# Kernel tuning notes

Hardware: AMD Instinct MI355X
Metric: run time of the kernel (lower is better)

The kernel has to match this reference:

```python
import jax, jax.numpy as jnp
import numpy as np

S, T, C, L_GNN, L_TF, H = 8, 16, 128, 3, 2, 4
B = 512
FF = 4 * C
EPS = 1e-5


def setup_inputs() -> dict:
    key = jax.random.key(0)
    ks = jax.random.split(key, 24)
    w = lambda k, shape: jax.random.normal(k, shape, jnp.float32) * 0.05
    inp = {}
    inp["xx"] = jax.random.randint(ks[0], (B, T, S, S, S), 0, 3, dtype=jnp.int32)
    inp["ss"] = jax.random.uniform(ks[1], (B, 1), jnp.float32)
    # DynamicGNNv2 params
    inp["Win"] = w(ks[2], (C, 5)); inp["b_in"] = w(ks[3], (C,))
    inp["Wl"] = w(ks[4], (L_GNN, C, C)); inp["bl"] = w(ks[5], (L_GNN, C))   # SAGEConv lin_l (neighbors)
    inp["Wr"] = w(ks[6], (L_GNN, C, C))                                      # SAGEConv lin_r (root, no bias)
    inp["ln_g"] = jnp.ones((C,), jnp.float32); inp["ln_b"] = jnp.zeros((C,), jnp.float32)  # shared LayerNorm
    # TransformerEncoder params (norm_first, relu, dropout=0 at eval)
    inp["Wqkv"] = w(ks[7], (L_TF, 3 * C, C)); inp["bqkv"] = w(ks[8], (L_TF, 3 * C))
    inp["Wo"] = w(ks[9], (L_TF, C, C)); inp["bo"] = w(ks[10], (L_TF, C))
    inp["ln1_g"] = jnp.ones((L_TF, C), jnp.float32); inp["ln1_b"] = jnp.zeros((L_TF, C), jnp.float32)
    inp["ln2_g"] = jnp.ones((L_TF, C), jnp.float32); inp["ln2_b"] = jnp.zeros((L_TF, C), jnp.float32)
    inp["W1"] = w(ks[11], (L_TF, FF, C)); inp["b1"] = w(ks[12], (L_TF, FF))
    inp["W2"] = w(ks[13], (L_TF, C, FF)); inp["b2"] = w(ks[14], (L_TF, C))
    inp["Wact"] = w(ks[15], (C, S ** 3)); inp["bact"] = w(ks[16], (C,))
    inp["Wsc"] = w(ks[17], (C, 1)); inp["bsc"] = w(ks[18], (C,))
    return inp


def layernorm(x, g, b):
    mu = x.mean(-1, keepdims=True)
    var = ((x - mu) ** 2).mean(-1, keepdims=True)
    return (x - mu) * jax.lax.rsqrt(var + EPS) * g + b


def reference(xx, ss, Win, b_in, Wl, bl, Wr, ln_g, ln_b, Wqkv, bqkv, Wo, bo,
              ln1_g, ln1_b, ln2_g, ln2_b, W1, b1, W2, b2, Wact, bact, Wsc, bsc):
    Bc = xx.shape[0]
    S3 = S ** 3
    frame0 = xx[:, 0].reshape(Bc, S3).astype(jnp.float32)            # (B,S^3)
    m = (frame0 != 0).astype(jnp.float32)                            # active-node mask
    grid = jnp.arange(S3)
    i, j, k = grid // (S * S), (grid // S) % S, grid % S
    coord = jnp.stack([i, j, k], -1).astype(jnp.float32) / (S - 1)   # (S^3,3)
    feat = jnp.concatenate([
        jnp.broadcast_to(coord, (Bc, S3, 3)),
        (frame0 / 2.0)[..., None],
        jnp.broadcast_to((ss / S)[:, None, :], (Bc, S3, 1)),
    ], -1)                                                            # (B,S^3,5)
    x = feat @ Win.T + b_in                                           # lin_in
    mm = m[..., None]
    n = m.sum(-1, keepdims=True)[..., None]                           # nodes per graph (B,1,1)
    for l in range(L_GNN):
        # complete graph (no self loops): mean over neighbors = (sum_active - self)/(N-1)
        s = (x * mm).sum(1, keepdims=True)                            # (B,1,C)
        neigh = jnp.where(n > 1, (s - x) / jnp.maximum(n - 1.0, 1.0), 0.0)
        h = neigh @ Wl[l].T + bl[l] + x @ Wr[l].T                     # SAGEConv
        x = layernorm(jax.nn.relu(h), ln_g, ln_b)
    full = x * mm                                                     # scatter-fill into dense (B,S^3,C)
    # pooling matmul: mean over each i/j/k slice -> (B,3S,C)
    poolW = jnp.concatenate([
        (i[None, :] == jnp.arange(S)[:, None]).astype(jnp.float32),
        (j[None, :] == jnp.arange(S)[:, None]).astype(jnp.float32),
        (k[None, :] == jnp.arange(S)[:, None]).astype(jnp.float32),
    ], 0)                                                             # (3S,S^3)
    gnn_emb = jnp.einsum('ps,bsc->bpc', poolW, full) / poolW.sum(1)[None, :, None]
    # transformer over past actions
    a = xx[:, 1:].reshape(Bc, T - 1, S3).astype(jnp.float32) @ Wact.T + bact
    Hd = C // H
    scale = 1.0 / np.sqrt(Hd).astype(np.float32)
    split_heads = lambda t: t.reshape(Bc, -1, H, Hd).transpose(0, 2, 1, 3)
    for l in range(L_TF):
        h1 = layernorm(a, ln1_g[l], ln1_b[l])
        q, kk, v = jnp.split(h1 @ Wqkv[l].T + bqkv[l], 3, axis=-1)
        q, kk, v = split_heads(q), split_heads(kk), split_heads(v)
        att = jax.nn.softmax(jnp.einsum('bhqd,bhkd->bhqk', q, kk) * scale, -1)
        o = jnp.einsum('bhqk,bhkd->bhqd', att, v).transpose(0, 2, 1, 3).reshape(Bc, -1, C)
        a = a + (o @ Wo[l].T + bo[l])
        h2 = layernorm(a, ln2_g[l], ln2_b[l])
        a = a + (jax.nn.relu(h2 @ W1[l].T + b1[l]) @ W2[l].T + b2[l])
    act_emb = a.mean(1)                                               # (B,C)
    mv_emb = jax.nn.relu(ss @ Wsc.T + bsc)                            # (B,C)
    return jnp.concatenate([gnn_emb, act_emb[:, None], mv_emb[:, None]], 1)  # (B,3S+2,C)
```

## Files before the change

kernel.cpp:

```cpp
#include <hip/hip_runtime.h>
#include <hip/hip_bf16.h>
#include <string.h>

typedef __hip_bfloat16 bf16;
typedef __attribute__((ext_vector_type(8))) short short8;
typedef __attribute__((ext_vector_type(4))) float f32x4;

#define Bsz 512
#define S3  512
#define Tsz 16
#define Cc  128
#define TT  15
#define XP  136
#define EPSv 1e-5f

__device__ __forceinline__ float u2f(unsigned short u) {
    return __uint_as_float(((unsigned)u) << 16);
}
__device__ __forceinline__ float ulo(unsigned u) { return __uint_as_float(u << 16); }
__device__ __forceinline__ float uhi(unsigned u) { return __uint_as_float(u & 0xffff0000u); }
__device__ __forceinline__ unsigned short f2bu(float v) {
    bf16 h = __float2bfloat16(v);
    unsigned short u; memcpy(&u, &h, 2); return u;
}
__device__ __forceinline__ unsigned short bfr16(float a) {
    unsigned u = __float_as_uint(a);
    u = u + 0x7fffu + ((u >> 16) & 1u);
    return (unsigned short)(u >> 16);
}
__device__ __forceinline__ unsigned fpack2(float a, float b) {
    unsigned r;
    asm("v_cvt_pk_bf16_f32 %0, %1, %2" : "=v"(r) : "v"(a), "v"(b));
    return r;
}
__device__ __forceinline__ float dot4(float4 a, float4 b) {
    return a.x*b.x + a.y*b.y + a.z*b.z + a.w*b.w;
}


__global__ __launch_bounds__(256) void k_tpack(const float* __restrict__ src,
                                               float* __restrict__ dst,
                                               int NR, int NK)
{
    __shared__ float tile[32][33];
    int k0 = blockIdx.x * 32, r0 = blockIdx.y * 32;
    int lr = threadIdx.x >> 5, lk = threadIdx.x & 31;
    for (int i = lr; i < 32; i += 8)
        tile[i][lk] = src[(size_t)(r0 + i) * NK + k0 + lk];
    __syncthreads();
    int c = threadIdx.x & 31, k4 = threadIdx.x >> 5;
    float4 v;
    v.x = tile[c][k4 * 4 + 0]; v.y = tile[c][k4 * 4 + 1];
    v.z = tile[c][k4 * 4 + 2]; v.w = tile[c][k4 * 4 + 3];
    ((float4*)dst)[(size_t)(k0 / 4 + k4) * NR + r0 + c] = v;
}

__global__ __launch_bounds__(256) void k_cvt5(
    const float* __restrict__ s0, const float* __restrict__ s1,
    const float* __restrict__ s2, const float* __restrict__ s3,
    const float* __restrict__ s4, ushort* __restrict__ dst)
{
    int i = blockIdx.x * 256 + threadIdx.x;
    if (i >= 114688) return;
    const float* src; int rel;
    if (i < 16384)      { src = s0; rel = i; }
    else if (i < 40960) { src = s1; rel = i - 16384; }
    else if (i < 49152) { src = s2; rel = i - 40960; }
    else if (i < 81920) { src = s3; rel = i - 49152; }
    else                { src = s4; rel = i - 81920; }
    float4 v = ((const float4*)src)[rel];
    ushort4 o;
    o.x = f2bu(v.x); o.y = f2bu(v.y); o.z = f2bu(v.z); o.w = f2bu(v.w);
    ((ushort4*)dst)[i] = o;
}

__global__ __launch_bounds__(256) void k_wpack(
    const float* __restrict__ Wl, const float* __restrict__ Wr,
    ushort* __restrict__ WB)
{
    int l = blockIdx.x, w = blockIdx.y;
    const float* src = (w == 0 ? Wl : Wr) + l * 16384;
    ushort* dst = WB + (size_t)(l * 2 + w) * 32 * 512;
    for (int item = threadIdx.x; item < 2048; item += 256) {
        int f = item >> 6, lane = item & 63;
        int t = f >> 2, ks = f & 3, ml = lane & 15, q = lane >> 4;
        int n = t * 16 + ml;
        const float* sA = src + n * 128 + 32 * ks + q * 4;
        const float* sB = sA + 16;
        float4 a = *(const float4*)sA;
        float4 b = *(const float4*)sB;
        ushort4 o0, o1;
        o0.x = f2bu(a.x); o0.y = f2bu(b.x); o0.z = f2bu(a.y); o0.w = f2bu(b.y);
        o1.x = f2bu(a.z); o1.y = f2bu(b.z); o1.z = f2bu(a.w); o1.w = f2bu(b.w);
        ushort* dp = dst + (size_t)f * 512 + lane * 8;
        *(ushort4*)dp = o0;
        *(ushort4*)(dp + 4) = o1;
    }
}

__global__ __launch_bounds__(512, 2) void k_torso(
    const int* __restrict__ xx, const float* __restrict__ ss,
    const float* __restrict__ Win, const float* __restrict__ b_in,
    const ushort* __restrict__ WB,
    const float4* __restrict__ WlP, const float* __restrict__ blv,
    const float* __restrict__ lng, const float* __restrict__ lnb,
    float* __restrict__ out)
{
    __shared__ ushort X[512 * XP];
    __shared__ ushort Ds[16 * 512];
    __shared__ ushort mCu[512];
    __shared__ float  sred[8 * 128];
    __shared__ float  ssc[128];
    __shared__ float  sbase[128];
    __shared__ float  gln[128], bln[128];
    __shared__ float  scnt[8];
    __shared__ float  invS;

    int b = blockIdx.x, tid = threadIdx.x;
    int wv = tid >> 6, lane = tid & 63;
    int ml = lane & 15, quad = lane >> 4;

    int* fC = (int*)Ds;

    const int* x0 = xx + (size_t)b * Tsz * S3;
    {
        int f0 = x0[tid];
        fC[tid] = f0;
        mCu[tid] = (f0 != 0) ? (ushort)0x3F80 : (ushort)0;
        unsigned long long bal = __ballot(f0 != 0);
        if (lane == 0) scnt[wv] = (float)__popcll(bal);
    }
    if (tid < 128) { gln[tid] = lng[tid]; bln[tid] = lnb[tid]; }
    __syncthreads();

    {
        int cp = lane;
        int co0 = 32 * (cp >> 4) + (cp & 15), co1 = co0 + 16;
        float f4c = ss[b] * (1.0f / 8.0f);
        float a0 = Win[co0*5+0], a1 = Win[co0*5+1], a2 = Win[co0*5+2], a3 = Win[co0*5+3];
        float c0 = Win[co1*5+0], c1 = Win[co1*5+1], c2 = Win[co1*5+2], c3 = Win[co1*5+3];
        float ba = b_in[co0] + f4c * Win[co0*5+4];
        float bc = b_in[co1] + f4c * Win[co1*5+4];
        float sp0 = 0.f, sp1 = 0.f;
        for (int node = wv; node < S3; node += 8) {
            int f0 = fC[node];
            float m = (f0 != 0) ? 1.f : 0.f;
            float ci = (float)(node >> 6) * (1.f / 7.f);
            float cj = (float)((node >> 3) & 7) * (1.f / 7.f);
            float ck = (float)(node & 7) * (1.f / 7.f);
            float ft = (float)f0 * 0.5f;
            float v0 = ba + ci * a0 + cj * a1 + ck * a2 + ft * a3;
            float v1 = bc + ci * c0 + cj * c1 + ck * c2 + ft * c3;
            ((unsigned*)(X + node * XP))[cp] = fpack2(v0, v1);
            sp0 += v0 * m; sp1 += v1 * m;
        }
        sred[wv * 128 + co0] = sp0;
        sred[wv * 128 + co1] = sp1;
    }
    __syncthreads();
    if (tid == 0) {
        float n = 0.f;
#pragma unroll
        for (int g = 0; g < 8; g++) n += scnt[g];
        invS = (n > 1.f) ? 1.f / (n - 1.f) : 0.f;
    }
    __syncthreads();
    if (tid < 128) {
        float s = 0.f;
#pragma unroll
        for (int g = 0; g < 8; g++) s += sred[g * 128 + tid];
        ssc[tid] = s * invS;
    }
    __syncthreads();
    {
        int part = tid >> 7, c = tid & 127;
        float a = 0.f;
#pragma unroll
        for (int k4 = part * 8; k4 < part * 8 + 8; k4++)
            a += dot4(*(const float4*)(ssc + k4 * 4), WlP[k4 * 384 + c]);
        sred[part * 128 + c] = a;
    }
    __syncthreads();
    if (tid < 128)
        sbase[tid] = blv[tid] + sred[tid] + sred[128 + tid] + sred[256 + tid] + sred[384 + tid];
    __syncthreads();

    float ninv = -invS;

#define D_BUILD(H)                                                            \
    {                                                                         \
        const ushort* wl = WB + ((size_t)(l * 2 + 0) * 32 + (H) * 16) * 512;  \
        const ushort* wr = WB + ((size_t)(l * 2 + 1) * 32 + (H) * 16) * 512;  \
        for (int g = tid; g < 1024; g += 512) {                               \
            uint4 ul = *(const uint4*)(wl + g * 8);                           \
            uint4 ur = *(const uint4*)(wr + g * 8);                           \
            uint4 d;                                                          \
            d.x = fpack2(fmaf(ninv, ulo(ul.x), ulo(ur.x)), fmaf(ninv, uhi(ul.x), uhi(ur.x))); \
            d.y = fpack2(fmaf(ninv, ulo(ul.y), ulo(ur.y)), fmaf(ninv, uhi(ul.y), uhi(ur.y))); \
            d.z = fpack2(fmaf(ninv, ulo(ul.z), ulo(ur.z)), fmaf(ninv, uhi(ul.z), uhi(ur.z))); \
            d.w = fpack2(fmaf(ninv, ulo(ul.w), ulo(ur.w)), fmaf(ninv, uhi(ul.w), uhi(ur.w))); \
            *(uint4*)(Ds + g * 8) = d;                                        \
        }                                                                     \
    }

#define GEMM_HALF(OFF)                                                        \
    _Pragma("unroll")                                                         \
    for (int ks = 0; ks < 4; ks++) {                                          \
        short8 a[4];                                                          \
        _Pragma("unroll")                                                     \
        for (int mm = 0; mm < 4; mm++)                                        \
            a[mm] = *(const short8*)(xrb + mm * 16 * XP + ks * 32);           \
        _Pragma("unroll")                                                     \
        for (int tq = 0; tq < 4; tq++) {                                      \
            short8 bg = *(const short8*)(Ds + (size_t)(tq * 4 + ks) * 512 + lane * 8); \
            _Pragma("unroll")                                                 \
            for (int mm = 0; mm < 4; mm++)                                    \
                acc[(OFF) + tq][mm] = __builtin_amdgcn_mfma_f32_16x16x32_bf16(a[mm], bg, acc[(OFF) + tq][mm], 0, 0, 0); \
        }                                                                     \
    }

    for (int l = 0; l < 3; l++) {
        bool last = (l == 2);
        float sp[8];
#pragma unroll
        for (int t = 0; t < 8; t++) sp[t] = 0.f;

        f32x4 acc[8][4];
#pragma unroll
        for (int t = 0; t < 8; t++)
#pragma unroll
            for (int mm = 0; mm < 4; mm++) acc[t][mm] = (f32x4){0.f, 0.f, 0.f, 0.f};

        const ushort* xrb = X + (wv * 64 + ml) * XP + quad * 8;

        D_BUILD(0); __syncthreads(); GEMM_HALF(0); __syncthreads();
        D_BUILD(1); __syncthreads(); GEMM_HALF(4); __syncthreads();

        float bse[8], gg[8], be[8];
#pragma unroll
        for (int t = 0; t < 8; t++) {
            bse[t] = sbase[t * 16 + ml];
            gg[t]  = gln[t * 16 + ml];
            be[t]  = bln[t * 16 + ml];
        }
#pragma unroll
        for (int mm = 0; mm < 4; mm++) {
#pragma unroll
            for (int r = 0; r < 4; r++) {
                int row = wv * 64 + mm * 16 + quad * 4 + r;
                float v[8];
                float s = 0.f, q = 0.f;
#pragma unroll
                for (int t = 0; t < 8; t++) {
                    float vv = fmaxf(acc[t][mm][r] + bse[t], 0.f);
                    v[t] = vv;
                    s += vv; q = fmaf(vv, vv, q);
                }
#pragma unroll
                for (int off = 1; off <= 8; off <<= 1) {
                    s += __shfl_xor(s, off, 64);
                    q += __shfl_xor(q, off, 64);
                }
                float mu = s * (1.f / 128.f);
                float rs = rsqrtf(q * (1.f / 128.f) - mu * mu + EPSv);
                float mrow = u2f(mCu[row]);
                unsigned* xr32 = (unsigned*)(X + row * XP);
                if (last) {
#pragma unroll
                    for (int t2 = 0; t2 < 4; t2++) {
                        float y0 = ((v[2*t2]   - mu) * rs * gg[2*t2]   + be[2*t2])   * mrow;
                        float y1 = ((v[2*t2+1] - mu) * rs * gg[2*t2+1] + be[2*t2+1]) * mrow;
                        xr32[t2 * 16 + ml] = fpack2(y0, y1);
                    }
                } else {
#pragma unroll
                    for (int t2 = 0; t2 < 4; t2++) {
                        float y0 = (v[2*t2]   - mu) * rs * gg[2*t2]   + be[2*t2];
                        float y1 = (v[2*t2+1] - mu) * rs * gg[2*t2+1] + be[2*t2+1];
                        sp[2*t2]   = fmaf(y0, mrow, sp[2*t2]);
                        sp[2*t2+1] = fmaf(y1, mrow, sp[2*t2+1]);
                        xr32[t2 * 16 + ml] = fpack2(y0, y1);
                    }
                }
            }
        }

        if (!last) {
#pragma unroll
            for (int t = 0; t < 8; t++) {
                sp[t] += __shfl_xor(sp[t], 16, 64);
                sp[t] += __shfl_xor(sp[t], 32, 64);
            }
            if (quad == 0) {
#pragma unroll
                for (int t = 0; t < 8; t++) sred[wv * 128 + t * 16 + ml] = sp[t];
            }
            __syncthreads();
            if (tid < 128) {
                float s = 0.f;
#pragma unroll
                for (int g = 0; g < 8; g++) s += sred[g * 128 + tid];
                ssc[tid] = s * invS;
            }
            __syncthreads();
            {
                int part = tid >> 7, c = tid & 127;
                float a = 0.f;
#pragma unroll
                for (int k4 = part * 8; k4 < part * 8 + 8; k4++)
                    a += dot4(*(const float4*)(ssc + k4 * 4), WlP[k4 * 384 + (l + 1) * 128 + c]);
                sred[part * 128 + c] = a;
            }
            __syncthreads();
            if (tid < 128)
                sbase[tid] = blv[(l + 1) * 128 + tid] + sred[tid] + sred[128 + tid] + sred[256 + tid] + sred[384 + tid];
            __syncthreads();
        }
    }
    __syncthreads();

    for (int item = tid; item < 768; item += 512) {
        int c4 = item & 31, p = item >> 5;
        int axis = p >> 3, idx = p & 7;
        float4 sum = {0.f, 0.f, 0.f, 0.f};
        for (int t = 0; t < 64; t++) {
            int node;
            if (axis == 0)      node = idx * 64 + t;
            else if (axis == 1) node = (t >> 3) * 64 + idx * 8 + (t & 7);
            else                node = t * 8 + idx;
            uint2 pk = *(const uint2*)(X + node * XP + c4 * 4);
            sum.x += ulo(pk.x);
            sum.y += uhi(pk.x);
            sum.z += ulo(pk.y);
            sum.w += uhi(pk.y);
        }
        int E0 = 32 * (c4 >> 3) + 2 * (c4 & 7);
        float* ob = out + (size_t)b * 26 * Cc + p * Cc;
        float2 lo = {sum.x * (1.f / 64.f), sum.z * (1.f / 64.f)};
        float2 hi = {sum.y * (1.f / 64.f), sum.w * (1.f / 64.f)};
        *(float2*)(ob + E0)      = lo;
        *(float2*)(ob + E0 + 16) = hi;
    }
}

__global__ __launch_bounds__(256) void k_tf3(
    const int* __restrict__ xx, const float* __restrict__ ss,
    const ushort* __restrict__ WactB, const float* __restrict__ bact,
    const ushort* __restrict__ WqkvB, const float* __restrict__ bqkv,
    const ushort* __restrict__ WoB, const float* __restrict__ bo,
    const float* __restrict__ ln1g, const float* __restrict__ ln1b,
    const float* __restrict__ ln2g, const float* __restrict__ ln2b,
    const ushort* __restrict__ W1B, const float* __restrict__ b1v,
    const ushort* __restrict__ W2B, const float* __restrict__ b2v,
    const float* __restrict__ Wsc, const float* __restrict__ bsc,
    float* __restrict__ out)
{
    __shared__ float  As[TT * 132];
    __shared__ ushort Qs[16 * 392];
    __shared__ ushort Ab[16 * 136];
    __shared__ ushort Hs[16 * 136];
    __shared__ ushort Fs[16 * 520];
    __shared__ float  Att[60 * 16];
    __shared__ float  mu_s[TT], rs_s[TT];

    int b = blockIdx.x, tid = threadIdx.x;
    int wv = tid >> 6, lane = tid & 63;
    int ml = lane & 15, quad = lane >> 4;

    const int* xa = xx + (size_t)b * Tsz * S3 + S3;
    for (int f = tid; f < TT * 512; f += 256) {
        int t = f >> 9, s = f & 511;
        Fs[t * 520 + s] = bfr16((float)xa[t * 512 + s]);
    }
    __syncthreads();

    {
        f32x4 acc[2];
#pragma unroll
        for (int i = 0; i < 2; i++) acc[i] = (f32x4){0.f, 0.f, 0.f, 0.f};
        const ushort* ar = Fs + ml * 520 + quad * 8;
        for (int ks = 0; ks < 16; ks++) {
            short8 a = *(const short8*)(ar + ks * 32);
#pragma unroll
            for (int i = 0; i < 2; i++) {
                int n0 = (wv * 2 + i) * 16;
                short8 bfr = *(const short8*)(WactB + (size_t)(n0 + ml) * 512 + quad * 8 + ks * 32);
                acc[i] = __builtin_amdgcn_mfma_f32_16x16x32_bf16(a, bfr, acc[i], 0, 0, 0);
            }
        }
#pragma unroll
        for (int i = 0; i < 2; i++) {
            int col = (wv * 2 + i) * 16 + ml;
            float bb = bact[col];
#pragma unroll
            for (int r = 0; r < 4; r++) {
                int row = quad * 4 + r;
                if (row < TT) As[row * 132 + col] = acc[i][r] + bb;
            }
        }
    }
    __syncthreads();

    for (int l = 0; l < 2; l++) {
        const float* bq  = bqkv + l * 384;
        const float* bol = bo + l * 128;
        const float* g1  = ln1g + l * 128; const float* be1 = ln1b + l * 128;
        const float* g2  = ln2g + l * 128; const float* be2 = ln2b + l * 128;
        const float* b1l = b1v + l * 512;  const float* b2l = b2v + l * 128;

        for (int r = wv; r < TT; r += 4) {
            float2 v = *(const float2*)(As + r * 132 + lane * 2);
            float s = v.x + v.y, q = v.x * v.x + v.y * v.y;
            for (int off = 32; off; off >>= 1) {
                s += __shfl_xor(s, off, 64);
                q += __shfl_xor(q, off, 64);
            }
            if (lane == 0) {
                float mu = s * (1.f / 128.f);
                mu_s[r] = mu;
                rs_s[r] = rsqrtf(q * (1.f / 128.f) - mu * mu + EPSv);
            }
        }
        __syncthreads();
        for (int f = tid; f < TT * 64; f += 256) {
            int t = f >> 6, cp = f & 63;
            float mu = mu_s[t], rs = rs_s[t];
            float x0 = (As[t * 132 + 2 * cp]     - mu) * rs * g1[2 * cp]     + be1[2 * cp];
            float x1 = (As[t * 132 + 2 * cp + 1] - mu) * rs * g1[2 * cp + 1] + be1[2 * cp + 1];
            ((unsigned*)(Ab + t * 136))[cp] = fpack2(x0, x1);
        }
        __syncthreads();

        {
            short8 a[4];
            const ushort* ar = Ab + ml * 136 + quad * 8;
#pragma unroll
            for (int ks = 0; ks < 4; ks++) a[ks] = *(const short8*)(ar + ks * 32);
#pragma unroll
            for (int i = 0; i < 6; i++) {
                int n0 = (wv * 6 + i) * 16;
                f32x4 acc = (f32x4){0.f, 0.f, 0.f, 0.f};
                const ushort* wb = WqkvB + (size_t)(l * 384 + n0 + ml) * 128 + quad * 8;
#pragma unroll
                for (int ks = 0; ks < 4; ks++) {
                    short8 bfr = *(const short8*)(wb + ks * 32);
                    acc = __builtin_amdgcn_mfma_f32_16x16x32_bf16(a[ks], bfr, acc, 0, 0, 0);
                }
                int col = n0 + ml;
                float bb = bq[col];
#pragma unroll
                for (int r = 0; r < 4; r++) {
                    int row = quad * 4 + r;
                    if (row < TT) Qs[row * 392 + col] = bfr16(acc[r] + bb);
                }
            }
        }
        __syncthreads();

        if (tid < 60) {
            int h = tid / 15, tq = tid % 15;
            const ushort* qp = Qs + tq * 392 + h * 32;
            float sc[TT];
            float mx = -1e30f;
#pragma unroll
            for (int tk = 0; tk < TT; tk++) {
                const ushort* kp = Qs + tk * 392 + 128 + h * 32;
                float d = 0.f;
#pragma unroll
                for (int u = 0; u < 32; u += 4) {
                    uint2 qa = *(const uint2*)(qp + u);
                    uint2 ka = *(const uint2*)(kp + u);
                    d += ulo(qa.x) * ulo(ka.x) + uhi(qa.x) * uhi(ka.x)
                       + ulo(qa.y) * ulo(ka.y) + uhi(qa.y) * uhi(ka.y);
                }
                d *= 0.17677669529663689f;
                sc[tk] = d; mx = fmaxf(mx, d);
            }
            float sum = 0.f;
#pragma unroll
            for (int tk = 0; tk < TT; tk++) { float e = __expf(sc[tk] - mx); sc[tk] = e; sum += e; }
            float r = 1.f / sum;
#pragma unroll
            for (int tk = 0; tk < TT; tk++) Att[tid * 16 + tk] = sc[tk] * r;
        }
        __syncthreads();

        for (int f = tid; f < TT * 64; f += 256) {
            int t = f >> 6, cp = f & 63;
            int h = cp >> 4;
            const float* ap = Att + (h * 15 + t) * 16;
            const ushort* vp = Qs + 256 + 2 * cp;
            float a0 = 0.f, a1 = 0.f;
#pragma unroll
            for (int tk = 0; tk < TT; tk++) {
                float w = ap[tk];
                unsigned pk = *(const unsigned*)(vp + tk * 392);
                a0 += w * ulo(pk);
                a1 += w * uhi(pk);
            }
            ((unsigned*)(Hs + t * 136))[cp] = fpack2(a0, a1);
        }
        __syncthreads();

        {
            short8 a[4];
            const ushort* ar = Hs + ml * 136 + quad * 8;
#pragma unroll
            for (int ks = 0; ks < 4; ks++) a[ks] = *(const short8*)(ar + ks * 32);
#pragma unroll
            for (int i = 0; i < 2; i++) {
                int n0 = (wv * 2 + i) * 16;
                f32x4 acc = (f32x4){0.f, 0.f, 0.f, 0.f};
                const ushort* wb = WoB + (size_t)(l * 128 + n0 + ml) * 128 + quad * 8;
#pragma unroll
                for (int ks = 0; ks < 4; ks++) {
                    short8 bfr = *(const short8*)(wb + ks * 32);
                    acc = __builtin_amdgcn_mfma_f32_16x16x32_bf16(a[ks], bfr, acc, 0, 0, 0);
                }
                int col = n0 + ml;
                float bb = bol[col];
#pragma unroll
                for (int r = 0; r < 4; r++) {
                    int row = quad * 4 + r;
                    if (row < TT) As[row * 132 + col] += acc[r] + bb;
                }
            }
        }
        __syncthreads();

        for (int r = wv; r < TT; r += 4) {
            float2 v = *(const float2*)(As + r * 132 + lane * 2);
            float s = v.x + v.y, q = v.x * v.x + v.y * v.y;
            for (int off = 32; off; off >>= 1) {
                s += __shfl_xor(s, off, 64);
                q += __shfl_xor(q, off, 64);
            }
            if (lane == 0) {
                float mu = s * (1.f / 128.f);
                mu_s[r] = mu;
                rs_s[r] = rsqrtf(q * (1.f / 128.f) - mu * mu + EPSv);
            }
        }
        __syncthreads();
        for (int f = tid; f < TT * 64; f += 256) {
            int t = f >> 6, cp = f & 63;
            float mu = mu_s[t], rs = rs_s[t];
            float x0 = (As[t * 132 + 2 * cp]     - mu) * rs * g2[2 * cp]     + be2[2 * cp];
            float x1 = (As[t * 132 + 2 * cp + 1] - mu) * rs * g2[2 * cp + 1] + be2[2 * cp + 1];
            ((unsigned*)(Ab + t * 136))[cp] = fpack2(x0, x1);
        }
        __syncthreads();

        {
            short8 a[4];
            const ushort* ar = Ab + ml * 136 + quad * 8;
#pragma unroll
            for (int ks = 0; ks < 4; ks++) a[ks] = *(const short8*)(ar + ks * 32);
#pragma unroll
            for (int i = 0; i < 8; i++) {
                int n0 = (wv * 8 + i) * 16;
                f32x4 acc = (f32x4){0.f, 0.f, 0.f, 0.f};
                const ushort* wb = W1B + (size_t)(l * 512 + n0 + ml) * 128 + quad * 8;
#pragma unroll
                for (int ks = 0; ks < 4; ks++) {
                    short8 bfr = *(const short8*)(wb + ks * 32);
                    acc = __builtin_amdgcn_mfma_f32_16x16x32_bf16(a[ks], bfr, acc, 0, 0, 0);
                }
                int col = n0 + ml;
                float bb = b1l[col];
#pragma unroll
                for (int r = 0; r < 4; r++) {
                    int row = quad * 4 + r;
                    if (row < TT) Fs[row * 520 + col] = bfr16(fmaxf(acc[r] + bb, 0.f));
                }
            }
        }
        __syncthreads();

        {
            f32x4 acc[2];
#pragma unroll
            for (int i = 0; i < 2; i++) acc[i] = (f32x4){0.f, 0.f, 0.f, 0.f};
            const ushort* ar = Fs + ml * 520 + quad * 8;
            for (int ks = 0; ks < 16; ks++) {
                short8 a = *(const short8*)(ar + ks * 32);
#pragma unroll
                for (int i = 0; i < 2; i++) {
                    int n0 = (wv * 2 + i) * 16;
                    short8 bfr = *(const short8*)(W2B + (size_t)(l * 128 + n0 + ml) * 512 + quad * 8 + ks * 32);
                    acc[i] = __builtin_amdgcn_mfma_f32_16x16x32_bf16(a, bfr, acc[i], 0, 0, 0);
                }
            }
#pragma unroll
            for (int i = 0; i < 2; i++) {
                int col = (wv * 2 + i) * 16 + ml;
                float bb = b2l[col];
#pragma unroll
                for (int r = 0; r < 4; r++) {
                    int row = quad * 4 + r;
                    if (row < TT) As[row * 132 + col] += acc[i][r] + bb;
                }
            }
        }
        __syncthreads();
    }

    if (tid < 128) {
        float s = 0.f;
#pragma unroll
        for (int t = 0; t < TT; t++) s += As[t * 132 + tid];
        out[(size_t)b * 26 * Cc + 24 * Cc + tid] = s * (1.f / 15.f);
    } else if (tid < 256) {
        int co = tid - 128;
        float v = ss[b] * Wsc[co] + bsc[co];
        out[(size_t)b * 26 * Cc + 25 * Cc + co] = fmaxf(v, 0.f);
    }
}

extern "C" void kernel_launch(void* const* d_in, const int* in_sizes, int n_in,
                              void* d_out, int out_size, void* d_ws, size_t ws_size,
                              hipStream_t stream)
{
    (void)in_sizes; (void)n_in; (void)out_size; (void)ws_size;
    const int*   xx   = (const int*)d_in[0];
    const float* ss   = (const float*)d_in[1];
    const float* Win  = (const float*)d_in[2];
    const float* b_in = (const float*)d_in[3];
    const float* Wl   = (const float*)d_in[4];
    const float* bl   = (const float*)d_in[5];
    const float* Wr   = (const float*)d_in[6];
    const float* lng  = (const float*)d_in[7];
    const float* lnb  = (const float*)d_in[8];
    const float* Wqkv = (const float*)d_in[9];
    const float* bqkv = (const float*)d_in[10];
    const float* Wo   = (const float*)d_in[11];
    const float* bo   = (const float*)d_in[12];
    const float* ln1g = (const float*)d_in[13];
    const float* ln1b = (const float*)d_in[14];
    const float* ln2g = (const float*)d_in[15];
    const float* ln2b = (const float*)d_in[16];
    const float* W1   = (const float*)d_in[17];
    const float* b1   = (const float*)d_in[18];
    const float* W2   = (const float*)d_in[19];
    const float* b2   = (const float*)d_in[20];
    const float* Wact = (const float*)d_in[21];
    const float* bact = (const float*)d_in[22];
    const float* Wsc  = (const float*)d_in[23];
    const float* bsc  = (const float*)d_in[24];
    float* out = (float*)d_out;

    char* ws = (char*)d_ws;
    size_t off = 0;
    float* WlT  = (float*)(ws + off); off += 384 * 128 * 4;
    ushort* WB    = (ushort*)(ws + off); off += (size_t)3 * 2 * 128 * 128 * 2;
    ushort* WactB = (ushort*)(ws + off); off += 128 * 512 * 2;
    ushort* WqkvB = (ushort*)(ws + off); off += 768 * 128 * 2;
    ushort* WoB   = (ushort*)(ws + off); off += 256 * 128 * 2;
    ushort* W1B   = (ushort*)(ws + off); off += 1024 * 128 * 2;
    ushort* W2B   = (ushort*)(ws + off); off += 256 * 512 * 2;

    k_tpack<<<dim3(4, 12), 256, 0, stream>>>(Wl, WlT, 384, 128);
    k_cvt5<<<448, 256, 0, stream>>>(Wact, Wqkv, Wo, W1, W2, WactB);
    k_wpack<<<dim3(3, 2), 256, 0, stream>>>(Wl, Wr, WB);

    k_torso<<<Bsz, 512, 0, stream>>>(xx, ss, Win, b_in, WB,
                                     (const float4*)WlT, bl, lng, lnb, out);

    k_tf3<<<Bsz, 256, 0, stream>>>(xx, ss,
                                   WactB, bact, WqkvB, bqkv, WoB, bo,
                                   ln1g, ln1b, ln2g, ln2b,
                                   W1B, b1, W2B, b2,
                                   Wsc, bsc, out);
}
```

Measured before the change: 287.2 us.

## Double torso block to 1024 threads and parallelize attention scores across lanes

The GNN torso kernel moves from 512 to 1024 threads per block, so each wave handles 32 rows instead of 64, with halved MFMA accumulators. The reduction scratch buffer is aliased into the Ds region to save LDS. In the transformer kernel, the input conversion is vectorized with int4 loads, and the attention score dot products are split four ways across lanes and combined with shuffles. The aim is more parallelism and latency hiding per block, in exchange for fewer blocks per CU and more barrier participants.

```diff
diff --git a/kernel.cpp b/kernel.cpp
--- a/kernel.cpp
+++ b/kernel.cpp
@@ -98,7 +98,7 @@
     }
 }
 
-__global__ __launch_bounds__(512, 2) void k_torso(
+__global__ __launch_bounds__(1024) void k_torso(
     const int* __restrict__ xx, const float* __restrict__ ss,
     const float* __restrict__ Win, const float* __restrict__ b_in,
     const ushort* __restrict__ WB,
@@ -109,7 +109,6 @@
     __shared__ ushort X[512 * XP];
     __shared__ ushort Ds[16 * 512];
     __shared__ ushort mCu[512];
-    __shared__ float  sred[8 * 128];
     __shared__ float  ssc[128];
     __shared__ float  sbase[128];
     __shared__ float  gln[128], bln[128];
@@ -120,10 +119,11 @@
     int wv = tid >> 6, lane = tid & 63;
     int ml = lane & 15, quad = lane >> 4;
 
-    int* fC = (int*)Ds;
+    int*   fC   = (int*)Ds;
+    float* sred = (float*)(Ds + 4096);
 
     const int* x0 = xx + (size_t)b * Tsz * S3;
-    {
+    if (tid < 512) {
         int f0 = x0[tid];
         fC[tid] = f0;
         mCu[tid] = (f0 != 0) ? (ushort)0x3F80 : (ushort)0;
@@ -142,7 +142,7 @@
         float ba = b_in[co0] + f4c * Win[co0*5+4];
         float bc = b_in[co1] + f4c * Win[co1*5+4];
         float sp0 = 0.f, sp1 = 0.f;
-        for (int node = wv; node < S3; node += 8) {
+        for (int node = wv; node < S3; node += 16) {
             int f0 = fC[node];
             float m = (f0 != 0) ? 1.f : 0.f;
             float ci = (float)(node >> 6) * (1.f / 7.f);
@@ -168,7 +168,7 @@
     if (tid < 128) {
         float s = 0.f;
 #pragma unroll
-        for (int g = 0; g < 8; g++) s += sred[g * 128 + tid];
+        for (int g = 0; g < 16; g++) s += sred[g * 128 + tid];
         ssc[tid] = s * invS;
     }
     __syncthreads();
@@ -176,13 +176,17 @@
         int part = tid >> 7, c = tid & 127;
         float a = 0.f;
 #pragma unroll
-        for (int k4 = part * 8; k4 < part * 8 + 8; k4++)
+        for (int k4 = part * 4; k4 < part * 4 + 4; k4++)
             a += dot4(*(const float4*)(ssc + k4 * 4), WlP[k4 * 384 + c]);
         sred[part * 128 + c] = a;
     }
     __syncthreads();
-    if (tid < 128)
-        sbase[tid] = blv[tid] + sred[tid] + sred[128 + tid] + sred[256 + tid] + sred[384 + tid];
+    if (tid < 128) {
+        float a = blv[tid];
+#pragma unroll
+        for (int p = 0; p < 8; p++) a += sred[p * 128 + tid];
+        sbase[tid] = a;
+    }
     __syncthreads();
 
     float ninv = -invS;
@@ -191,31 +195,30 @@
     {                                                                         \
         const ushort* wl = WB + ((size_t)(l * 2 + 0) * 32 + (H) * 16) * 512;  \
         const ushort* wr = WB + ((size_t)(l * 2 + 1) * 32 + (H) * 16) * 512;  \
-        for (int g = tid; g < 1024; g += 512) {                               \
-            uint4 ul = *(const uint4*)(wl + g * 8);                           \
-            uint4 ur = *(const uint4*)(wr + g * 8);                           \
-            uint4 d;                                                          \
-            d.x = fpack2(fmaf(ninv, ulo(ul.x), ulo(ur.x)), fmaf(ninv, uhi(ul.x), uhi(ur.x))); \
-            d.y = fpack2(fmaf(ninv, ulo(ul.y), ulo(ur.y)), fmaf(ninv, uhi(ul.y), uhi(ur.y))); \
-            d.z = fpack2(fmaf(ninv, ulo(ul.z), ulo(ur.z)), fmaf(ninv, uhi(ul.z), uhi(ur.z))); \
-            d.w = fpack2(fmaf(ninv, ulo(ul.w), ulo(ur.w)), fmaf(ninv, uhi(ul.w), uhi(ur.w))); \
-            *(uint4*)(Ds + g * 8) = d;                                        \
-        }                                                                     \
+        int g = tid;                                                          \
+        uint4 ul = *(const uint4*)(wl + g * 8);                               \
+        uint4 ur = *(const uint4*)(wr + g * 8);                               \
+        uint4 d;                                                              \
+        d.x = fpack2(fmaf(ninv, ulo(ul.x), ulo(ur.x)), fmaf(ninv, uhi(ul.x), uhi(ur.x))); \
+        d.y = fpack2(fmaf(ninv, ulo(ul.y), ulo(ur.y)), fmaf(ninv, uhi(ul.y), uhi(ur.y))); \
+        d.z = fpack2(fmaf(ninv, ulo(ul.z), ulo(ur.z)), fmaf(ninv, uhi(ul.z), uhi(ur.z))); \
+        d.w = fpack2(fmaf(ninv, ulo(ul.w), ulo(ur.w)), fmaf(ninv, uhi(ul.w), uhi(ur.w))); \
+        *(uint4*)(Ds + g * 8) = d;                                            \
     }
 
 #define GEMM_HALF(OFF)                                                        \
     _Pragma("unroll")                                                         \
     for (int ks = 0; ks < 4; ks++) {                                          \
-        short8 a[4];                                                          \
+        short8 a0 = *(const short8*)(xr0 + ks * 32);                          \
+        short8 a1 = *(const short8*)(xr1 + ks * 32);                          \
+        short8 bg[4];                                                         \
         _Pragma("unroll")                                                     \
-        for (int mm = 0; mm < 4; mm++)                                        \
-            a[mm] = *(const short8*)(xrb + mm * 16 * XP + ks * 32);           \
+        for (int t = 0; t < 4; t++)                                           \
+            bg[t] = *(const short8*)(Ds + (size_t)(t * 4 + ks) * 512 + lane * 8); \
         _Pragma("unroll")                                                     \
-        for (int tq = 0; tq < 4; tq++) {                                      \
-            short8 bg = *(const short8*)(Ds + (size_t)(tq * 4 + ks) * 512 + lane * 8); \
-            _Pragma("unroll")                                                 \
-            for (int mm = 0; mm < 4; mm++)                                    \
-                acc[(OFF) + tq][mm] = __builtin_amdgcn_mfma_f32_16x16x32_bf16(a[mm], bg, acc[(OFF) + tq][mm], 0, 0, 0); \
+        for (int t = 0; t < 4; t++) {                                         \
+            acc[(OFF) + t][0] = __builtin_amdgcn_mfma_f32_16x16x32_bf16(a0, bg[t], acc[(OFF) + t][0], 0, 0, 0); \
+            acc[(OFF) + t][1] = __builtin_amdgcn_mfma_f32_16x16x32_bf16(a1, bg[t], acc[(OFF) + t][1], 0, 0, 0); \
         }                                                                     \
     }
 
@@ -225,13 +228,14 @@
 #pragma unroll
         for (int t = 0; t < 8; t++) sp[t] = 0.f;
 
-        f32x4 acc[8][4];
+        f32x4 acc[8][2];
 #pragma unroll
         for (int t = 0; t < 8; t++)
 #pragma unroll
-            for (int mm = 0; mm < 4; mm++) acc[t][mm] = (f32x4){0.f, 0.f, 0.f, 0.f};
-
-        const ushort* xrb = X + (wv * 64 + ml) * XP + quad * 8;
+            for (int mm = 0; mm < 2; mm++) acc[t][mm] = (f32x4){0.f, 0.f, 0.f, 0.f};
+
+        const ushort* xr0 = X + (wv * 32 + ml) * XP + quad * 8;
+        const ushort* xr1 = xr0 + 16 * XP;
 
         D_BUILD(0); __syncthreads(); GEMM_HALF(0); __syncthreads();
         D_BUILD(1); __syncthreads(); GEMM_HALF(4); __syncthreads();
@@ -244,16 +248,15 @@
             be[t]  = bln[t * 16 + ml];
         }
 #pragma unroll
-        for (int mm = 0; mm < 4; mm++) {
+        for (int mm = 0; mm < 2; mm++) {
 #pragma unroll
             for (int r = 0; r < 4; r++) {
-                int row = wv * 64 + mm * 16 + quad * 4 + r;
-                float v[8];
+                int row = wv * 32 + mm * 16 + quad * 4 + r;
                 float s = 0.f, q = 0.f;
 #pragma unroll
                 for (int t = 0; t < 8; t++) {
                     float vv = fmaxf(acc[t][mm][r] + bse[t], 0.f);
-                    v[t] = vv;
+                    acc[t][mm][r] = vv;
                     s += vv; q = fmaf(vv, vv, q);
                 }
 #pragma unroll
@@ -268,15 +271,15 @@
                 if (last) {
 #pragma unroll
                     for (int t2 = 0; t2 < 4; t2++) {
-                        float y0 = ((v[2*t2]   - mu) * rs * gg[2*t2]   + be[2*t2])   * mrow;
-                        float y1 = ((v[2*t2+1] - mu) * rs * gg[2*t2+1] + be[2*t2+1]) * mrow;
+                        float y0 = ((acc[2*t2][mm][r]   - mu) * rs * gg[2*t2]   + be[2*t2])   * mrow;
+                        float y1 = ((acc[2*t2+1][mm][r] - mu) * rs * gg[2*t2+1] + be[2*t2+1]) * mrow;
                         xr32[t2 * 16 + ml] = fpack2(y0, y1);
                     }
                 } else {
 #pragma unroll
                     for (int t2 = 0; t2 < 4; t2++) {
-                        float y0 = (v[2*t2]   - mu) * rs * gg[2*t2]   + be[2*t2];
-                        float y1 = (v[2*t2+1] - mu) * rs * gg[2*t2+1] + be[2*t2+1];
+                        float y0 = (acc[2*t2][mm][r]   - mu) * rs * gg[2*t2]   + be[2*t2];
+                        float y1 = (acc[2*t2+1][mm][r] - mu) * rs * gg[2*t2+1] + be[2*t2+1];
                         sp[2*t2]   = fmaf(y0, mrow, sp[2*t2]);
                         sp[2*t2+1] = fmaf(y1, mrow, sp[2*t2+1]);
                         xr32[t2 * 16 + ml] = fpack2(y0, y1);
@@ -299,7 +302,7 @@
             if (tid < 128) {
                 float s = 0.f;
 #pragma unroll
-                for (int g = 0; g < 8; g++) s += sred[g * 128 + tid];
+                for (int g = 0; g < 16; g++) s += sred[g * 128 + tid];
                 ssc[tid] = s * invS;
             }
             __syncthreads();
@@ -307,20 +310,24 @@
                 int part = tid >> 7, c = tid & 127;
                 float a = 0.f;
 #pragma unroll
-                for (int k4 = part * 8; k4 < part * 8 + 8; k4++)
+                for (int k4 = part * 4; k4 < part * 4 + 4; k4++)
                     a += dot4(*(const float4*)(ssc + k4 * 4), WlP[k4 * 384 + (l + 1) * 128 + c]);
                 sred[part * 128 + c] = a;
             }
             __syncthreads();
-            if (tid < 128)
-                sbase[tid] = blv[(l + 1) * 128 + tid] + sred[tid] + sred[128 + tid] + sred[256 + tid] + sred[384 + tid];
+            if (tid < 128) {
+                float a = blv[(l + 1) * 128 + tid];
+#pragma unroll
+                for (int p = 0; p < 8; p++) a += sred[p * 128 + tid];
+                sbase[tid] = a;
+            }
             __syncthreads();
         }
     }
     __syncthreads();
 
-    for (int item = tid; item < 768; item += 512) {
-        int c4 = item & 31, p = item >> 5;
+    if (tid < 768) {
+        int c4 = tid & 31, p = tid >> 5;
         int axis = p >> 3, idx = p & 7;
         float4 sum = {0.f, 0.f, 0.f, 0.f};
         for (int t = 0; t < 64; t++) {
@@ -368,9 +375,16 @@
     int ml = lane & 15, quad = lane >> 4;
 
     const int* xa = xx + (size_t)b * Tsz * S3 + S3;
-    for (int f = tid; f < TT * 512; f += 256) {
-        int t = f >> 9, s = f & 511;
-        Fs[t * 520 + s] = bfr16((float)xa[t * 512 + s]);
+    {
+        const int4* xa4 = (const int4*)xa;
+        for (int i = tid; i < 1920; i += 256) {
+            int4 v = xa4[i];
+            int t = i >> 7, s = (i & 127) << 2;
+            ushort4 o;
+            o.x = bfr16((float)v.x); o.y = bfr16((float)v.y);
+            o.z = bfr16((float)v.z); o.w = bfr16((float)v.w);
+            *(ushort4*)(Fs + t * 520 + s) = o;
+        }
     }
     __syncthreads();
 
@@ -457,31 +471,37 @@
         }
         __syncthreads();
 
-        if (tid < 60) {
-            int h = tid / 15, tq = tid % 15;
-            const ushort* qp = Qs + tq * 392 + h * 32;
+        if (tid < 240) {
+            int pair = tid >> 2, part = tid & 3;
+            int h = pair / 15, tq = pair % 15;
+            const ushort* qp = Qs + tq * 392 + h * 32 + part * 8;
             float sc[TT];
-            float mx = -1e30f;
 #pragma unroll
             for (int tk = 0; tk < TT; tk++) {
-                const ushort* kp = Qs + tk * 392 + 128 + h * 32;
-                float d = 0.f;
-#pragma unroll
-                for (int u = 0; u < 32; u += 4) {
-                    uint2 qa = *(const uint2*)(qp + u);
-                    uint2 ka = *(const uint2*)(kp + u);
-                    d += ulo(qa.x) * ulo(ka.x) + uhi(qa.x) * uhi(ka.x)
-                       + ulo(qa.y) * ulo(ka.y) + uhi(qa.y) * uhi(ka.y);
-                }
-                d *= 0.17677669529663689f;
-                sc[tk] = d; mx = fmaxf(mx, d);
-            }
-            float sum = 0.f;
-#pragma unroll
-            for (int tk = 0; tk < TT; tk++) { float e = __expf(sc[tk] - mx); sc[tk] = e; sum += e; }
-            float r = 1.f / sum;
-#pragma unroll
-            for (int tk = 0; tk < TT; tk++) Att[tid * 16 + tk] = sc[tk] * r;
+                const ushort* kp = Qs + tk * 392 + 128 + h * 32 + part * 8;
+                uint2 qa = *(const uint2*)(qp);
+                uint2 qb = *(const uint2*)(qp + 4);
+                uint2 ka = *(const uint2*)(kp);
+                uint2 kb = *(const uint2*)(kp + 4);
+                float d = ulo(qa.x) * ulo(ka.x) + uhi(qa.x) * uhi(ka.x)
+                        + ulo(qa.y) * ulo(ka.y) + uhi(qa.y) * uhi(ka.y)
+                        + ulo(qb.x) * ulo(kb.x) + uhi(qb.x) * uhi(kb.x)
+                        + ulo(qb.y) * ulo(kb.y) + uhi(qb.y) * uhi(kb.y);
+                d += __shfl_xor(d, 1, 64);
+                d += __shfl_xor(d, 2, 64);
+                sc[tk] = d * 0.17677669529663689f;
+            }
+            if (part == 0) {
+                float mx = -1e30f;
+#pragma unroll
+                for (int tk = 0; tk < TT; tk++) mx = fmaxf(mx, sc[tk]);
+                float sum = 0.f;
+#pragma unroll
+                for (int tk = 0; tk < TT; tk++) { float e = __expf(sc[tk] - mx); sc[tk] = e; sum += e; }
+                float r = 1.f / sum;
+#pragma unroll
+                for (int tk = 0; tk < TT; tk++) Att[pair * 16 + tk] = sc[tk] * r;
+            }
         }
         __syncthreads();
 
@@ -663,8 +683,8 @@
     k_cvt5<<<448, 256, 0, stream>>>(Wact, Wqkv, Wo, W1, W2, WactB);
     k_wpack<<<dim3(3, 2), 256, 0, stream>>>(Wl, Wr, WB);
 
-    k_torso<<<Bsz, 512, 0, stream>>>(xx, ss, Win, b_in, WB,
-                                     (const float4*)WlT, bl, lng, lnb, out);
+    k_torso<<<Bsz, 1024, 0, stream>>>(xx, ss, Win, b_in, WB,
+                                      (const float4*)WlT, bl, lng, lnb, out);
 
     k_tf3<<<Bsz, 256, 0, stream>>>(xx, ss,
                                    WactB, bact, WqkvB, bqkv, WoB, bo,
```

New measurement: 283.4 us. Within noise of the previous version (-1.3%).
